# Performance work log

Measured on AMD Instinct MI355X. Metric: run time of the kernel, lower is better.

## Reference

```python
import jax, jax.numpy as jnp
import numpy as np

N, STATE_DIM, HID, D_EMB, K = 8192, 512, 128, 128, 10
EPS = 0.001


def setup_inputs() -> dict:
    key = jax.random.key(0)
    ks = jax.random.split(key, 5)
    sc = lambda fan_in: 1.0 / np.sqrt(fan_in)
    return {
        "s": jax.random.normal(ks[0], (N, STATE_DIM), dtype=jnp.float32),
        "W1": jax.random.normal(ks[1], (HID, STATE_DIM), dtype=jnp.float32) * sc(STATE_DIM),
        "b1": jax.random.normal(ks[2], (HID,), dtype=jnp.float32) * sc(STATE_DIM),
        "W2": jax.random.normal(ks[3], (D_EMB, HID), dtype=jnp.float32) * sc(HID),
        "b2": jax.random.normal(ks[4], (D_EMB,), dtype=jnp.float32) * sc(HID),
        "k": K,
    }


def reference(s, W1, b1, W2, b2, k):
    # embedding: relu(Linear) -> Linear
    x = jax.nn.relu(s @ W1.T + b1) @ W2.T + b2            # [N, d_emb]
    # pairwise L2 distance matrix: ||xi||^2 + ||xj||^2 - 2 xi.xj
    sq = jnp.sum(x * x, axis=1)                            # [N]
    dist2 = sq[:, None] + sq[None, :] - 2.0 * (x @ x.T)    # [N, N]
    # clamp tiny negative values from cancellation (torch.sqrt would NaN)
    dist = jnp.sqrt(jnp.maximum(dist2, 1e-12))             # [N, N]
    # k nearest per row, excluding self (smallest entry = own distance ~0)
    neg_vals, _ = jax.lax.top_k(-dist, k + 1)              # [N, k+1], ascending dist
    k_nearest = -neg_vals[:, 1:]                           # [N, k]
    sum_k_nearest = jnp.sum(k_nearest, axis=1, keepdims=True)  # [N, 1]
    mean_k_nearest_2 = jnp.mean(sum_k_nearest) ** 2
    return EPS / (sum_k_nearest ** 2 / mean_k_nearest_2 + EPS)
```

## Files before the change

kernel.cpp:

```cpp
#include <hip/hip_runtime.h>
#include <hip/hip_bf16.h>

#define NN 8192
#define SD 512
#define HID 128
#define DE 128
#define KP1 11
#define EPSF 0.001f
#define NSPLIT 16
#define NCHUNK NSPLIT
#define TILE 32
#define NTILE ((NN / NSPLIT) / TILE)

using short8 = __attribute__((ext_vector_type(8))) short;
using f32x4 = __attribute__((ext_vector_type(4))) float;

__device__ inline ushort f2bf(float f) {
    __hip_bfloat16 b = __float2bfloat16(f);
    return *reinterpret_cast<ushort*>(&b);
}
__device__ inline float bf2f(ushort u) {
    unsigned v = (unsigned)u << 16;
    union { unsigned u; float f; } c; c.u = v; return c.f;
}

__global__ __launch_bounds__(256) void wsplit_kernel(
    const float* __restrict__ W1, const float* __restrict__ W2,
    ushort* __restrict__ W1h, ushort* __restrict__ W1l,
    ushort* __restrict__ W2h, ushort* __restrict__ W2l)
{
    const int bid = blockIdx.x;
    const float* src; ushort *dh, *dl; int base;
    if (bid < 64) { src = W1; dh = W1h; dl = W1l; base = bid * 1024; }
    else          { src = W2; dh = W2h; dl = W2l; base = (bid - 64) * 1024; }
    const int i = base + threadIdx.x * 4;
    float4 f = *reinterpret_cast<const float4*>(src + i);
    ushort h[4], lo[4];
    float fv[4] = {f.x, f.y, f.z, f.w};
#pragma unroll
    for (int j = 0; j < 4; ++j) {
        h[j] = f2bf(fv[j]);
        lo[j] = f2bf(fv[j] - bf2f(h[j]));
    }
    *reinterpret_cast<uint2*>(dh + i) = *reinterpret_cast<uint2*>(h);
    *reinterpret_cast<uint2*>(dl + i) = *reinterpret_cast<uint2*>(lo);
}

__global__ __launch_bounds__(256) void mlp_kernel(
    const float* __restrict__ s, const ushort* __restrict__ W1h,
    const ushort* __restrict__ W1l, const float* __restrict__ b1,
    const ushort* __restrict__ W2h, const ushort* __restrict__ W2l,
    const float* __restrict__ b2, __hip_bfloat16* __restrict__ xb,
    float* __restrict__ sqb)
{
    __shared__ __align__(16) ushort sbh[2][32 * 32];
    __shared__ __align__(16) ushort sbl[2][32 * 32];
    __shared__ __align__(16) ushort hbh[32 * 128];
    __shared__ __align__(16) ushort hbl[32 * 128];
    __shared__ __align__(16) ushort xtile[32 * 128];
    __shared__ float sqpart[4 * 32];

    const int t = threadIdx.x;
    const int w = t >> 6, l = t & 63;
    const int lc = l & 15, c4 = l >> 4;
    const int rb = blockIdx.x * 32;
    const int cb = w * 32;

    const int srow = t >> 3, skq = t & 7;
    const int ssl = ((skq >> 1) + (srow >> 2)) & 3;
    const int sByte = srow * 64 + (ssl ^ (srow & 3)) * 16 + (skq & 1) * 8;
    const float* sgbase = s + (size_t)(rb + srow) * SD + skq * 4;

    float4 sf;
#define STAGE_LOAD_S(kt_) sf = *reinterpret_cast<const float4*>(sgbase + (kt_) * 32)
#define STAGE_WRITE_S(b_) do { \
    float fv_[4] = {sf.x, sf.y, sf.z, sf.w}; \
    ushort h_[4], lo_[4]; \
    _Pragma("unroll") \
    for (int j_ = 0; j_ < 4; ++j_) { \
        h_[j_] = f2bf(fv_[j_]); \
        lo_[j_] = f2bf(fv_[j_] - bf2f(h_[j_])); \
    } \
    *reinterpret_cast<uint2*>(reinterpret_cast<char*>(sbh[b_]) + sByte) = *reinterpret_cast<uint2*>(h_); \
    *reinterpret_cast<uint2*>(reinterpret_cast<char*>(sbl[b_]) + sByte) = *reinterpret_cast<uint2*>(lo_); \
} while (0)

    int aByte[2];
#pragma unroll
    for (int rt = 0; rt < 2; ++rt) {
        int row = rt * 16 + lc;
        int sl = ((c4 + (row >> 2)) & 3) ^ (row & 3);
        aByte[rt] = row * 64 + sl * 16;
    }

    const ushort* w1hp[2]; const ushort* w1lp[2];
#pragma unroll
    for (int ct = 0; ct < 2; ++ct) {
        int col = cb + ct * 16 + lc;
        w1hp[ct] = W1h + (size_t)col * SD + c4 * 8;
        w1lp[ct] = W1l + (size_t)col * SD + c4 * 8;
    }

    f32x4 acc1[2][2];
#pragma unroll
    for (int rt = 0; rt < 2; ++rt)
#pragma unroll
        for (int ct = 0; ct < 2; ++ct) acc1[rt][ct] = {0.f, 0.f, 0.f, 0.f};

    STAGE_LOAD_S(0);
    STAGE_WRITE_S(0);
    short8 bh[2], bl[2], nbh[2], nbl[2];
#pragma unroll
    for (int ct = 0; ct < 2; ++ct) {
        bh[ct] = *reinterpret_cast<const short8*>(w1hp[ct]);
        bl[ct] = *reinterpret_cast<const short8*>(w1lp[ct]);
    }

    for (int kt = 0; kt < 16; ++kt) {
        __syncthreads();
        if (kt < 15) STAGE_LOAD_S(kt + 1);
        short8 ah[2], al[2];
#pragma unroll
        for (int rt = 0; rt < 2; ++rt) {
            ah[rt] = *reinterpret_cast<const short8*>(
                reinterpret_cast<char*>(sbh[kt & 1]) + aByte[rt]);
            al[rt] = *reinterpret_cast<const short8*>(
                reinterpret_cast<char*>(sbl[kt & 1]) + aByte[rt]);
        }
        if (kt < 15) {
#pragma unroll
            for (int ct = 0; ct < 2; ++ct) {
                nbh[ct] = *reinterpret_cast<const short8*>(w1hp[ct] + (kt + 1) * 32);
                nbl[ct] = *reinterpret_cast<const short8*>(w1lp[ct] + (kt + 1) * 32);
            }
        }
#pragma unroll
        for (int rt = 0; rt < 2; ++rt)
#pragma unroll
            for (int ct = 0; ct < 2; ++ct) {
                acc1[rt][ct] = __builtin_amdgcn_mfma_f32_16x16x32_bf16(ah[rt], bh[ct], acc1[rt][ct], 0, 0, 0);
                acc1[rt][ct] = __builtin_amdgcn_mfma_f32_16x16x32_bf16(ah[rt], bl[ct], acc1[rt][ct], 0, 0, 0);
                acc1[rt][ct] = __builtin_amdgcn_mfma_f32_16x16x32_bf16(al[rt], bh[ct], acc1[rt][ct], 0, 0, 0);
            }
        if (kt < 15) {
            STAGE_WRITE_S((kt + 1) & 1);
#pragma unroll
            for (int ct = 0; ct < 2; ++ct) { bh[ct] = nbh[ct]; bl[ct] = nbl[ct]; }
        }
    }

    float b1v[2];
#pragma unroll
    for (int ct = 0; ct < 2; ++ct) b1v[ct] = b1[cb + ct * 16 + lc];
#pragma unroll
    for (int rt = 0; rt < 2; ++rt)
#pragma unroll
        for (int ct = 0; ct < 2; ++ct)
#pragma unroll
            for (int reg = 0; reg < 4; ++reg) {
                float v = fmaxf(acc1[rt][ct][reg] + b1v[ct], 0.f);
                ushort hh = f2bf(v);
                ushort hl = f2bf(v - bf2f(hh));
                int row = rt * 16 + c4 * 4 + reg;
                int kcol = cb + ct * 16 + lc;
                int sl = (kcol >> 3) ^ (row & 15);
                int byte = row * 256 + sl * 16 + (kcol & 7) * 2;
                *reinterpret_cast<ushort*>(reinterpret_cast<char*>(hbh) + byte) = hh;
                *reinterpret_cast<ushort*>(reinterpret_cast<char*>(hbl) + byte) = hl;
            }
    __syncthreads();

    f32x4 acc2[2][2];
#pragma unroll
    for (int rt = 0; rt < 2; ++rt)
#pragma unroll
        for (int ct = 0; ct < 2; ++ct) acc2[rt][ct] = {0.f, 0.f, 0.f, 0.f};

#pragma unroll
    for (int kt = 0; kt < 4; ++kt) {
        short8 ah[2], al[2];
#pragma unroll
        for (int rt = 0; rt < 2; ++rt) {
            int row = rt * 16 + lc;
            int sl = (kt * 4 + c4) ^ (row & 15);
            int byte = row * 256 + sl * 16;
            ah[rt] = *reinterpret_cast<const short8*>(reinterpret_cast<char*>(hbh) + byte);
            al[rt] = *reinterpret_cast<const short8*>(reinterpret_cast<char*>(hbl) + byte);
        }
        short8 wh[2], wl[2];
#pragma unroll
        for (int ct = 0; ct < 2; ++ct) {
            int col = cb + ct * 16 + lc;
            wh[ct] = *reinterpret_cast<const short8*>(W2h + (size_t)col * HID + kt * 32 + c4 * 8);
            wl[ct] = *reinterpret_cast<const short8*>(W2l + (size_t)col * HID + kt * 32 + c4 * 8);
        }
#pragma unroll
        for (int rt = 0; rt < 2; ++rt)
#pragma unroll
            for (int ct = 0; ct < 2; ++ct) {
                acc2[rt][ct] = __builtin_amdgcn_mfma_f32_16x16x32_bf16(ah[rt], wh[ct], acc2[rt][ct], 0, 0, 0);
                acc2[rt][ct] = __builtin_amdgcn_mfma_f32_16x16x32_bf16(ah[rt], wl[ct], acc2[rt][ct], 0, 0, 0);
                acc2[rt][ct] = __builtin_amdgcn_mfma_f32_16x16x32_bf16(al[rt], wh[ct], acc2[rt][ct], 0, 0, 0);
            }
    }

    float b2v[2];
#pragma unroll
    for (int ct = 0; ct < 2; ++ct) b2v[ct] = b2[cb + ct * 16 + lc];
    float p[8];
#pragma unroll
    for (int j = 0; j < 8; ++j) p[j] = 0.f;
#pragma unroll
    for (int rt = 0; rt < 2; ++rt)
#pragma unroll
        for (int ct = 0; ct < 2; ++ct)
#pragma unroll
            for (int reg = 0; reg < 4; ++reg) {
                float v = acc2[rt][ct][reg] + b2v[ct];
                ushort xv = f2bf(v);
                float xf = bf2f(xv);
                p[rt * 4 + reg] = fmaf(xf, xf, p[rt * 4 + reg]);
                int row = rt * 16 + c4 * 4 + reg;
                int e = cb + ct * 16 + lc;
                xtile[row * 128 + e] = xv;
            }
#pragma unroll
    for (int j = 0; j < 8; ++j) {
#pragma unroll
        for (int off = 8; off >= 1; off >>= 1) p[j] += __shfl_xor(p[j], off, 16);
    }
    if (lc == 0) {
#pragma unroll
        for (int rt = 0; rt < 2; ++rt)
#pragma unroll
            for (int reg = 0; reg < 4; ++reg)
                sqpart[w * 32 + rt * 16 + c4 * 4 + reg] = p[rt * 4 + reg];
    }
    __syncthreads();
    if (t < 32)
        sqb[rb + t] = sqpart[t] + sqpart[32 + t] + sqpart[64 + t] + sqpart[96 + t];
    const short8* xsv = reinterpret_cast<const short8*>(xtile);
    short8* xg = reinterpret_cast<short8*>(reinterpret_cast<ushort*>(xb) + (size_t)rb * DE);
    xg[t] = xsv[t];
    xg[t + 256] = xsv[t + 256];
}

__global__ __launch_bounds__(256, 6) void knn_kernel(
    const ushort* __restrict__ xs, const float* __restrict__ sqb,
    float* __restrict__ part)
{
    __shared__ __align__(16) ushort lbuf[2][TILE * DE];

    const int bid = blockIdx.x;
    const int rid = bid >> 4, cid = bid & 15;
    const int t = threadIdx.x;
    const int w = t >> 6, l = t & 63;
    const int q16 = l & 15, lg = l >> 4;
    const int q = rid * 64 + w * 16 + q16;
    const int kk = lg * 8;
    const int cstart = cid * (NN / NSPLIT);

    short8 bq[4];
#pragma unroll
    for (int kb = 0; kb < 4; ++kb)
        bq[kb] = *reinterpret_cast<const short8*>(xs + (size_t)q * DE + kb * 32 + kk);

    float m[KP1];
#pragma unroll
    for (int j = 0; j < KP1; ++j) m[j] = 1e30f;

    auto ins = [&](float d2) {
#pragma unroll
        for (int j = KP1 - 1; j >= 1; --j)
            m[j] = __builtin_amdgcn_fmed3f(d2, m[j - 1], m[j]);
        m[0] = fminf(d2, m[0]);
    };

    const int s0 = t, s1 = t + 256;
    const int g0 = (s0 >> 4) * DE + (s0 & 15) * 8;
    const int g1 = (s1 >> 4) * DE + (s1 & 15) * 8;
    const int d0 = ((s0 >> 4) * 16 + ((s0 & 15) ^ ((s0 >> 4) & 7))) * 8;
    const int d1 = ((s1 >> 4) * 16 + ((s1 & 15) ^ ((s1 >> 4) & 7))) * 8;

    short8 vS0, vS1;
#define STAGE_LOAD(tt_) do { \
    const ushort* sb_ = xs + (size_t)(cstart + (tt_) * TILE) * DE; \
    vS0 = *reinterpret_cast<const short8*>(sb_ + g0); \
    vS1 = *reinterpret_cast<const short8*>(sb_ + g1); \
} while (0)
#define STAGE_WRITE(nb_) do { \
    *reinterpret_cast<short8*>(&lbuf[nb_][d0]) = vS0; \
    *reinterpret_cast<short8*>(&lbuf[nb_][d1]) = vS1; \
} while (0)

    STAGE_LOAD(0);
    STAGE_WRITE(0);

    for (int tt = 0; tt < NTILE; ++tt) {
        __syncthreads();
        if (tt + 1 < NTILE) STAGE_LOAD(tt + 1);

        const int c0 = cstart + tt * TILE;
        float4 sv0 = *reinterpret_cast<const float4*>(sqb + c0 + lg * 4);
        float4 sv1 = *reinterpret_cast<const float4*>(sqb + c0 + 16 + lg * 4);

        const ushort* lb = lbuf[tt & 1];
        short8 fa[4], fb[4];
#pragma unroll
        for (int kb = 0; kb < 4; ++kb) {
            int col = (kb * 4 + lg) ^ (q16 & 7);
            fa[kb] = *reinterpret_cast<const short8*>(lb + (q16 * 16 + col) * 8);
            fb[kb] = *reinterpret_cast<const short8*>(lb + ((16 + q16) * 16 + col) * 8);
        }
        f32x4 acc0 = {0.f, 0.f, 0.f, 0.f}, acc1 = {0.f, 0.f, 0.f, 0.f};
#pragma unroll
        for (int kb = 0; kb < 4; ++kb) {
            acc0 = __builtin_amdgcn_mfma_f32_16x16x32_bf16(fa[kb], bq[kb], acc0, 0, 0, 0);
            acc1 = __builtin_amdgcn_mfma_f32_16x16x32_bf16(fb[kb], bq[kb], acc1, 0, 0, 0);
        }
        ins(fmaf(-2.f, acc0[0], sv0.x));
        ins(fmaf(-2.f, acc0[1], sv0.y));
        ins(fmaf(-2.f, acc0[2], sv0.z));
        ins(fmaf(-2.f, acc0[3], sv0.w));
        ins(fmaf(-2.f, acc1[0], sv1.x));
        ins(fmaf(-2.f, acc1[1], sv1.y));
        ins(fmaf(-2.f, acc1[2], sv1.z));
        ins(fmaf(-2.f, acc1[3], sv1.w));

        if (tt + 1 < NTILE) STAGE_WRITE((tt + 1) & 1);
    }
#undef STAGE_LOAD
#undef STAGE_WRITE

    __syncthreads();
    float* mb = reinterpret_cast<float*>(lbuf);
#pragma unroll
    for (int j = 0; j < KP1; ++j)
        mb[((w * 4 + lg) * KP1 + j) * 16 + q16] = m[j];
    __syncthreads();
    if (lg == 0) {
#pragma unroll
        for (int g = 1; g < 4; ++g)
#pragma unroll
            for (int j = 0; j < KP1; ++j)
                ins(mb[((w * 4 + g) * KP1 + j) * 16 + q16]);
#pragma unroll
        for (int j = 0; j < KP1; ++j)
            part[(size_t)(cid * KP1 + j) * NN + q] = m[j];
    }
}

__global__ __launch_bounds__(256) void merge_kernel(
    const float* __restrict__ part, const float* __restrict__ sqb,
    float* __restrict__ sumk, float* __restrict__ psum)
{
    const int row = blockIdx.x * 256 + threadIdx.x;
    float m[KP1];
#pragma unroll
    for (int j = 0; j < KP1; ++j) m[j] = 1e30f;
#pragma unroll
    for (int ch = 0; ch < NCHUNK; ++ch) {
#pragma unroll
        for (int j = 0; j < KP1; ++j) {
            float d2 = part[(size_t)(ch * KP1 + j) * NN + row];
#pragma unroll
            for (int jj = KP1 - 1; jj >= 1; --jj)
                m[jj] = __builtin_amdgcn_fmed3f(d2, m[jj - 1], m[jj]);
            m[0] = fminf(d2, m[0]);
        }
    }
    const float sqq = sqb[row];
    float sum = 0.f;
#pragma unroll
    for (int j = 1; j < KP1; ++j)
        sum += sqrtf(fmaxf(m[j] + sqq, 1e-12f));
    sumk[row] = sum;

    float p = sum;
#pragma unroll
    for (int off = 32; off >= 1; off >>= 1) p += __shfl_xor(p, off, 64);
    __shared__ float red[4];
    if ((threadIdx.x & 63) == 0) red[threadIdx.x >> 6] = p;
    __syncthreads();
    if (threadIdx.x == 0) psum[blockIdx.x] = red[0] + red[1] + red[2] + red[3];
}

__global__ void reduce_kernel(const float* __restrict__ psum, float* __restrict__ qv)
{
    const int t = threadIdx.x;
    float p = (t < 32) ? psum[t] : 0.f;
#pragma unroll
    for (int off = 32; off >= 1; off >>= 1) p += __shfl_xor(p, off, 64);
    if (t == 0) {
        float mean = p * (1.0f / NN);
        qv[0] = EPSF * mean * mean;
    }
}

__global__ __launch_bounds__(256) void final_kernel(
    const float* __restrict__ sumk, const float* __restrict__ qv,
    float* __restrict__ out)
{
    const int i = blockIdx.x * 256 + threadIdx.x;
    const float qq = qv[0];
    const float sv = sumk[i];
    out[i] = qq / (fmaf(sv, sv, qq));
}

extern "C" void kernel_launch(void* const* d_in, const int* in_sizes, int n_in,
                              void* d_out, int out_size, void* d_ws, size_t ws_size,
                              hipStream_t stream)
{
    const float* s  = (const float*)d_in[0];
    const float* W1 = (const float*)d_in[1];
    const float* b1 = (const float*)d_in[2];
    const float* W2 = (const float*)d_in[3];
    const float* b2 = (const float*)d_in[4];
    float* out = (float*)d_out;

    char* ws = (char*)d_ws;
    __hip_bfloat16* xb = (__hip_bfloat16*)ws;
    float* sqb  = (float*)(ws + (size_t)NN * DE * 2);
    float* part = sqb + NN;
    float* sumk = part + (size_t)NCHUNK * KP1 * NN;
    float* psum = sumk + NN;
    float* qv   = psum + 32;
    ushort* W1h = (ushort*)(qv + 1);
    ushort* W1l = W1h + (size_t)HID * SD;
    ushort* W2h = W1l + (size_t)HID * SD;
    ushort* W2l = W2h + (size_t)DE * HID;

    wsplit_kernel<<<80, 256, 0, stream>>>(W1, W2, W1h, W1l, W2h, W2l);
    mlp_kernel<<<NN / 32, 256, 0, stream>>>(s, W1h, W1l, b1, W2h, W2l, b2, xb, sqb);
    knn_kernel<<<(NN / 64) * NSPLIT, 256, 0, stream>>>((const ushort*)xb, sqb, part);
    merge_kernel<<<NN / 256, 256, 0, stream>>>(part, sqb, sumk, psum);
    reduce_kernel<<<1, 64, 0, stream>>>(psum, qv);
    final_kernel<<<NN / 256, 256, 0, stream>>>(sumk, qv, out);
}
```

Measured before the change: 85.77 us.

## Double queries per wave and enlarge candidate tile in knn kernel

Each wave now handles 32 query rows (two 16-row MFMA B operands) instead of 16, so each candidate fragment read from LDS feeds two MFMAs. The candidate tile grows from 32 to 64 rows and the column squared norms are staged once into shared memory instead of being read from global memory every tile. The grid is halved to match, and the final per-wave merge covers both query sets. The aim is to cut LDS and global traffic per distance computed, at the cost of more registers, more LDS, fewer blocks and no occupancy hint in the launch bounds.

```diff
diff --git a/kernel.cpp b/kernel.cpp
--- a/kernel.cpp
+++ b/kernel.cpp
@@ -9,7 +9,7 @@
 #define EPSF 0.001f
 #define NSPLIT 16
 #define NCHUNK NSPLIT
-#define TILE 32
+#define TILE 64
 #define NTILE ((NN / NSPLIT) / TILE)
 
 using short8 = __attribute__((ext_vector_type(8))) short;
@@ -245,52 +245,72 @@
     xg[t + 256] = xsv[t + 256];
 }
 
-__global__ __launch_bounds__(256, 6) void knn_kernel(
+__global__ __launch_bounds__(256) void knn_kernel(
     const ushort* __restrict__ xs, const float* __restrict__ sqb,
     float* __restrict__ part)
 {
     __shared__ __align__(16) ushort lbuf[2][TILE * DE];
+    __shared__ __align__(16) float sqs[NN / NSPLIT];
 
     const int bid = blockIdx.x;
     const int rid = bid >> 4, cid = bid & 15;
     const int t = threadIdx.x;
     const int w = t >> 6, l = t & 63;
     const int q16 = l & 15, lg = l >> 4;
-    const int q = rid * 64 + w * 16 + q16;
     const int kk = lg * 8;
+    const int qb = rid * 128 + w * 32;
     const int cstart = cid * (NN / NSPLIT);
 
-    short8 bq[4];
+    short8 bq[2][4];
+#pragma unroll
+    for (int qs = 0; qs < 2; ++qs)
+#pragma unroll
+        for (int kb = 0; kb < 4; ++kb)
+            bq[qs][kb] = *reinterpret_cast<const short8*>(
+                xs + (size_t)(qb + qs * 16 + q16) * DE + kb * 32 + kk);
+
+    float m[2][KP1];
+#pragma unroll
+    for (int qs = 0; qs < 2; ++qs)
+#pragma unroll
+        for (int j = 0; j < KP1; ++j) m[qs][j] = 1e30f;
+
+#define INS(qs_, v_) do { \
+    float d2_ = (v_); \
+    _Pragma("unroll") \
+    for (int j_ = KP1 - 1; j_ >= 1; --j_) \
+        m[qs_][j_] = __builtin_amdgcn_fmed3f(d2_, m[qs_][j_ - 1], m[qs_][j_]); \
+    m[qs_][0] = fminf(d2_, m[qs_][0]); \
+} while (0)
+
+    if (t < 128)
+        reinterpret_cast<float4*>(sqs)[t] =
+            reinterpret_cast<const float4*>(sqb + cstart)[t];
+
+    int gIdx[4], dIdx[4];
+#pragma unroll
+    for (int i = 0; i < 4; ++i) {
+        int sl = t + 256 * i;
+        int row = sl >> 4, col = sl & 15;
+        gIdx[i] = row * DE + col * 8;
+        dIdx[i] = (row * 16 + (col ^ (row & 7))) * 8;
+    }
+    int aIdx[4];
 #pragma unroll
     for (int kb = 0; kb < 4; ++kb)
-        bq[kb] = *reinterpret_cast<const short8*>(xs + (size_t)q * DE + kb * 32 + kk);
-
-    float m[KP1];
-#pragma unroll
-    for (int j = 0; j < KP1; ++j) m[j] = 1e30f;
-
-    auto ins = [&](float d2) {
-#pragma unroll
-        for (int j = KP1 - 1; j >= 1; --j)
-            m[j] = __builtin_amdgcn_fmed3f(d2, m[j - 1], m[j]);
-        m[0] = fminf(d2, m[0]);
-    };
-
-    const int s0 = t, s1 = t + 256;
-    const int g0 = (s0 >> 4) * DE + (s0 & 15) * 8;
-    const int g1 = (s1 >> 4) * DE + (s1 & 15) * 8;
-    const int d0 = ((s0 >> 4) * 16 + ((s0 & 15) ^ ((s0 >> 4) & 7))) * 8;
-    const int d1 = ((s1 >> 4) * 16 + ((s1 & 15) ^ ((s1 >> 4) & 7))) * 8;
-
-    short8 vS0, vS1;
+        aIdx[kb] = (q16 * 16 + ((kb * 4 + lg) ^ (q16 & 7))) * 8;
+
+    short8 st[4];
 #define STAGE_LOAD(tt_) do { \
     const ushort* sb_ = xs + (size_t)(cstart + (tt_) * TILE) * DE; \
-    vS0 = *reinterpret_cast<const short8*>(sb_ + g0); \
-    vS1 = *reinterpret_cast<const short8*>(sb_ + g1); \
+    _Pragma("unroll") \
+    for (int i_ = 0; i_ < 4; ++i_) \
+        st[i_] = *reinterpret_cast<const short8*>(sb_ + gIdx[i_]); \
 } while (0)
 #define STAGE_WRITE(nb_) do { \
-    *reinterpret_cast<short8*>(&lbuf[nb_][d0]) = vS0; \
-    *reinterpret_cast<short8*>(&lbuf[nb_][d1]) = vS1; \
+    _Pragma("unroll") \
+    for (int i_ = 0; i_ < 4; ++i_) \
+        *reinterpret_cast<short8*>(&lbuf[nb_][dIdx[i_]]) = st[i_]; \
 } while (0)
 
     STAGE_LOAD(0);
@@ -299,54 +319,60 @@
     for (int tt = 0; tt < NTILE; ++tt) {
         __syncthreads();
         if (tt + 1 < NTILE) STAGE_LOAD(tt + 1);
-
-        const int c0 = cstart + tt * TILE;
-        float4 sv0 = *reinterpret_cast<const float4*>(sqb + c0 + lg * 4);
-        float4 sv1 = *reinterpret_cast<const float4*>(sqb + c0 + 16 + lg * 4);
-
         const ushort* lb = lbuf[tt & 1];
-        short8 fa[4], fb[4];
-#pragma unroll
-        for (int kb = 0; kb < 4; ++kb) {
-            int col = (kb * 4 + lg) ^ (q16 & 7);
-            fa[kb] = *reinterpret_cast<const short8*>(lb + (q16 * 16 + col) * 8);
-            fb[kb] = *reinterpret_cast<const short8*>(lb + ((16 + q16) * 16 + col) * 8);
-        }
-        f32x4 acc0 = {0.f, 0.f, 0.f, 0.f}, acc1 = {0.f, 0.f, 0.f, 0.f};
-#pragma unroll
-        for (int kb = 0; kb < 4; ++kb) {
-            acc0 = __builtin_amdgcn_mfma_f32_16x16x32_bf16(fa[kb], bq[kb], acc0, 0, 0, 0);
-            acc1 = __builtin_amdgcn_mfma_f32_16x16x32_bf16(fb[kb], bq[kb], acc1, 0, 0, 0);
-        }
-        ins(fmaf(-2.f, acc0[0], sv0.x));
-        ins(fmaf(-2.f, acc0[1], sv0.y));
-        ins(fmaf(-2.f, acc0[2], sv0.z));
-        ins(fmaf(-2.f, acc0[3], sv0.w));
-        ins(fmaf(-2.f, acc1[0], sv1.x));
-        ins(fmaf(-2.f, acc1[1], sv1.y));
-        ins(fmaf(-2.f, acc1[2], sv1.z));
-        ins(fmaf(-2.f, acc1[3], sv1.w));
-
+#pragma unroll
+        for (int cs = 0; cs < 4; ++cs) {
+            short8 fa[4];
+#pragma unroll
+            for (int kb = 0; kb < 4; ++kb)
+                fa[kb] = *reinterpret_cast<const short8*>(lb + cs * 2048 + aIdx[kb]);
+            float4 sv = *reinterpret_cast<const float4*>(sqs + tt * TILE + cs * 16 + lg * 4);
+#pragma unroll
+            for (int qs = 0; qs < 2; ++qs) {
+                f32x4 acc = {0.f, 0.f, 0.f, 0.f};
+#pragma unroll
+                for (int kb = 0; kb < 4; ++kb)
+                    acc = __builtin_amdgcn_mfma_f32_16x16x32_bf16(fa[kb], bq[qs][kb], acc, 0, 0, 0);
+                INS(qs, fmaf(-2.f, acc[0], sv.x));
+                INS(qs, fmaf(-2.f, acc[1], sv.y));
+                INS(qs, fmaf(-2.f, acc[2], sv.z));
+                INS(qs, fmaf(-2.f, acc[3], sv.w));
+            }
+        }
         if (tt + 1 < NTILE) STAGE_WRITE((tt + 1) & 1);
     }
 #undef STAGE_LOAD
 #undef STAGE_WRITE
+#undef INS
 
     __syncthreads();
     float* mb = reinterpret_cast<float*>(lbuf);
 #pragma unroll
-    for (int j = 0; j < KP1; ++j)
-        mb[((w * 4 + lg) * KP1 + j) * 16 + q16] = m[j];
+    for (int qs = 0; qs < 2; ++qs)
+#pragma unroll
+        for (int j = 0; j < KP1; ++j)
+            mb[(((w * 2 + qs) * 4 + lg) * KP1 + j) * 16 + q16] = m[qs][j];
     __syncthreads();
-    if (lg == 0) {
+    if (l < 32) {
+        const int qs = l >> 4, qq = l & 15;
+        float mm[KP1];
+#pragma unroll
+        for (int j = 0; j < KP1; ++j)
+            mm[j] = mb[(((w * 2 + qs) * 4 + 0) * KP1 + j) * 16 + qq];
 #pragma unroll
         for (int g = 1; g < 4; ++g)
 #pragma unroll
-            for (int j = 0; j < KP1; ++j)
-                ins(mb[((w * 4 + g) * KP1 + j) * 16 + q16]);
+            for (int j = 0; j < KP1; ++j) {
+                float d2 = mb[(((w * 2 + qs) * 4 + g) * KP1 + j) * 16 + qq];
+#pragma unroll
+                for (int jj = KP1 - 1; jj >= 1; --jj)
+                    mm[jj] = __builtin_amdgcn_fmed3f(d2, mm[jj - 1], mm[jj]);
+                mm[0] = fminf(d2, mm[0]);
+            }
+        const int q = qb + qs * 16 + qq;
 #pragma unroll
         for (int j = 0; j < KP1; ++j)
-            part[(size_t)(cid * KP1 + j) * NN + q] = m[j];
+            part[(size_t)(cid * KP1 + j) * NN + q] = mm[j];
     }
 }
 
@@ -432,7 +458,7 @@
 
     wsplit_kernel<<<80, 256, 0, stream>>>(W1, W2, W1h, W1l, W2h, W2l);
     mlp_kernel<<<NN / 32, 256, 0, stream>>>(s, W1h, W1l, b1, W2h, W2l, b2, xb, sqb);
-    knn_kernel<<<(NN / 64) * NSPLIT, 256, 0, stream>>>((const ushort*)xb, sqb, part);
+    knn_kernel<<<(NN / 128) * NSPLIT, 256, 0, stream>>>((const ushort*)xb, sqb, part);
     merge_kernel<<<NN / 256, 256, 0, stream>>>(part, sqb, sumk, psum);
     reduce_kernel<<<1, 64, 0, stream>>>(psum, qv);
     final_kernel<<<NN / 256, 256, 0, stream>>>(sumk, qv, out);
```

Result: faster. 79.53 us (-7.3%).
